# Performance work log

Hardware: AMD Instinct MI355X
Metric: run time of the kernel (lower is better)

The kernel has to match this reference:

```python
import jax, jax.numpy as jnp
import numpy as np

B, S, D = 2, 2048, 3584
H, KV, HD = 28, 4, 128
N_REP = H // KV          # 7
MAX_S = 2048
SCALE = HD ** -0.5
ROPE_BASE = 1_000_000.0  # Qwen2 rope theta


def _rope_tables(max_s, hd, base):
    inv = 1.0 / (base ** (np.arange(0, hd, 2, dtype=np.float32) / hd))  # [hd/2]
    ang = np.arange(max_s, dtype=np.float32)[:, None] * inv[None, :]    # [S, hd/2]
    return jnp.asarray(np.cos(ang)), jnp.asarray(np.sin(ang))


def apply_rotary(x, cos, sin):
    # x: [b, s, h, hd] with interleaved complex pairs (torch view_as_complex layout)
    xr = x[..., 0::2]
    xi = x[..., 1::2]
    cos = cos[None, :, None, :]
    sin = sin[None, :, None, :]
    yr = xr * cos - xi * sin
    yi = xr * sin + xi * cos
    return jnp.stack([yr, yi], axis=-1).reshape(x.shape)


def setup_inputs() -> dict:
    key = jax.random.key(0)
    ks = jax.random.split(key, 8)
    w = 0.02
    x = jax.random.normal(ks[0], (B, S, D), jnp.float32)
    wq_w = jax.random.normal(ks[1], (H * HD, D), jnp.float32) * w
    wq_b = jax.random.normal(ks[2], (H * HD,), jnp.float32) * w
    wk_w = jax.random.normal(ks[3], (KV * HD, D), jnp.float32) * w
    wk_b = jax.random.normal(ks[4], (KV * HD,), jnp.float32) * w
    wv_w = jax.random.normal(ks[5], (KV * HD, D), jnp.float32) * w
    wv_b = jax.random.normal(ks[6], (KV * HD,), jnp.float32) * w
    wo_w = jax.random.normal(ks[7], (D, H * HD), jnp.float32) * w
    k_cache = jnp.zeros((B, MAX_S, KV, HD), jnp.float32)
    v_cache = jnp.zeros((B, MAX_S, KV, HD), jnp.float32)
    freqs_cos, freqs_sin = _rope_tables(MAX_S, HD, ROPE_BASE)
    # causal additive mask [s, t]; large-negative instead of -inf for safe grads
    mask = jnp.triu(jnp.full((S, S), -1e9, jnp.float32), k=1)
    return {"x": x, "wq_w": wq_w, "wq_b": wq_b, "wk_w": wk_w, "wk_b": wk_b,
            "wv_w": wv_w, "wv_b": wv_b, "wo_w": wo_w,
            "k_cache": k_cache, "v_cache": v_cache,
            "freqs_cos": freqs_cos, "freqs_sin": freqs_sin,
            "mask": mask, "start_pos": 0}


def reference(x, wq_w, wq_b, wk_w, wk_b, wv_w, wv_b, wo_w,
              k_cache, v_cache, freqs_cos, freqs_sin, mask, start_pos):
    bsz, seqlen, _ = x.shape
    end_pos = start_pos + seqlen
    q = (x @ wq_w.T + wq_b).reshape(bsz, seqlen, H, HD)
    k = (x @ wk_w.T + wk_b).reshape(bsz, seqlen, KV, HD)
    v = (x @ wv_w.T + wv_b).reshape(bsz, seqlen, KV, HD)
    cos = jax.lax.dynamic_slice_in_dim(freqs_cos, start_pos, seqlen, 0)
    sin = jax.lax.dynamic_slice_in_dim(freqs_sin, start_pos, seqlen, 0)
    q = apply_rotary(q, cos, sin)
    k = apply_rotary(k, cos, sin)
    # KV-cache write
    k_cache = jax.lax.dynamic_update_slice(k_cache, k, (0, start_pos, 0, 0))
    v_cache = jax.lax.dynamic_update_slice(v_cache, v, (0, start_pos, 0, 0))
    keys = k_cache[:bsz, :end_pos]    # [b, t, kv, hd]
    values = v_cache[:bsz, :end_pos]
    # GQA: repeat_interleave kv heads to n_heads
    keys = jnp.repeat(keys, N_REP, axis=2)      # [b, t, h, hd]
    values = jnp.repeat(values, N_REP, axis=2)
    scores = jnp.einsum('bshd,bthd->bsht', q, keys) * SCALE
    scores = scores + mask[None, :, None, :]
    probs = jax.nn.softmax(scores.astype(jnp.float32), axis=-1).astype(x.dtype)
    out = jnp.einsum('bsht,bthd->bshd', probs, values)
    out = out.reshape(bsz, seqlen, H * HD)
    return out @ wo_w.T
```

## Files before the change

### kernel.cpp

```cpp
#include <hip/hip_runtime.h>
#include <hip/hip_bf16.h>

typedef __attribute__((ext_vector_type(4)))  float  f32x4;
typedef __attribute__((ext_vector_type(16))) float  f32x16;
typedef __attribute__((ext_vector_type(8)))  __bf16 bf16x8;
typedef __attribute__((ext_vector_type(4)))  __bf16 bf16x4;
typedef __attribute__((ext_vector_type(4)))  unsigned int u32x4;

constexpr int S_LEN = 2048, DMODEL = 3584, NH = 28, NKV = 4, HD = 128, NREP = 7;
constexpr float SCALE_LOG2 = 0.1275174331f;

__device__ __forceinline__ unsigned int pack2(float a, float b) {
  unsigned short ua = __builtin_bit_cast(unsigned short, (__bf16)a);
  unsigned short ub = __builtin_bit_cast(unsigned short, (__bf16)b);
  return (unsigned int)ua | ((unsigned int)ub << 16);
}

__global__ void cvt_kernel(const float* __restrict__ in, __bf16* __restrict__ out, int n4) {
  int i = blockIdx.x * blockDim.x + threadIdx.x;
  if (i >= n4) return;
  float4 v = reinterpret_cast<const float4*>(in)[i];
  bf16x4 o;
  o[0] = (__bf16)v.x; o[1] = (__bf16)v.y; o[2] = (__bf16)v.z; o[3] = (__bf16)v.w;
  reinterpret_cast<bf16x4*>(out)[i] = o;
}

#define GLDS16(gsrc, ldst)                                                              \
  __builtin_amdgcn_global_load_lds((const __attribute__((address_space(1))) void*)(gsrc),\
                                   (__attribute__((address_space(3))) void*)(ldst), 16, 0, 0)

template <int MODE>
__global__ __launch_bounds__(512, 2) void gemm256(
    const __bf16* __restrict__ A, const __bf16* __restrict__ Bw,
    const float* __restrict__ bias, void* __restrict__ Cout,
    int M, int N, int K,
    const float* __restrict__ fcos, const float* __restrict__ fsin,
    const int* __restrict__ sp_ptr, float scale)
{
  extern __shared__ char smem[];
  const int tid = threadIdx.x;
  const int lane = tid & 63, wid = tid >> 6;
  const int wm = wid >> 2, wn = wid & 3;
  const int l15 = lane & 15, g = (lane >> 4) & 3;

  const int chunk = gridDim.x >> 3;
  const int wg = (blockIdx.x & 7) * chunk + (blockIdx.x >> 3);
  const int nbx = N >> 8;
  const int by = wg / nbx, bx = wg % nbx;
  const int row0 = by * 256, col0 = bx * 256;

  const int srL   = 16 * (tid >> 6) + ((tid >> 2) & 15);
  const int cperm = ((tid & 3) * 8) ^ (((tid >> 5) & 1) * 16);
  const __bf16* pA0 = A + (size_t)(row0 + srL) * K + cperm;
  const __bf16* pA1 = pA0 + (size_t)128 * K;
  const __bf16* pB0 = Bw + (size_t)(col0 + srL) * K + cperm;
  const __bf16* pB1 = pB0 + (size_t)128 * K;
  char* ldsA = smem + tid * 16;
  char* ldsB = smem + 65536 + tid * 16;

  const int sw = ((l15 >> 3) & 1) << 5;
  const int aoff = wm * 8192 + l15 * 64 + ((g * 16) ^ sw);
  const int boff = 65536 + wn * 4096 + l15 * 64 + ((g * 16) ^ sw);

  f32x4 acc[8][4] = {};
  const int nt = K >> 5;

#pragma unroll
  for (int pt = 0; pt < 3; pt++) {
    const size_t ko = (size_t)pt * 32;
    char* sA = ldsA + pt * 16384;
    char* sB = ldsB + pt * 16384;
    GLDS16(pA0 + ko, sA);
    GLDS16(pA1 + ko, sA + 8192);
    GLDS16(pB0 + ko, sB);
    GLDS16(pB1 + ko, sB + 8192);
  }
  asm volatile("s_waitcnt vmcnt(8)" ::: "memory");
  __builtin_amdgcn_s_barrier();
  __builtin_amdgcn_sched_barrier(0);

  for (int t = 0; t < nt; t++) {
    const int slot = (t & 3) * 16384;
    const char* sa = smem + slot + aoff;
    const char* sb = smem + slot + boff;
    bf16x8 af[4], bfv[4];

#pragma unroll
    for (int fm = 0; fm < 4; fm++)
      af[fm] = *reinterpret_cast<const bf16x8*>(sa + fm * 1024);
#pragma unroll
    for (int fn = 0; fn < 4; fn++)
      bfv[fn] = *reinterpret_cast<const bf16x8*>(sb + fn * 1024);
    if (t + 3 < nt) {
      const size_t ko = (size_t)(t + 3) * 32;
      char* sA = ldsA + ((t + 3) & 3) * 16384;
      GLDS16(pA0 + ko, sA);
      GLDS16(pA1 + ko, sA + 8192);
    }
    asm volatile("s_waitcnt lgkmcnt(0)" ::: "memory");
    __builtin_amdgcn_sched_barrier(0);
    __builtin_amdgcn_s_setprio(1);
#pragma unroll
    for (int fn = 0; fn < 4; fn++)
#pragma unroll
      for (int fm = 0; fm < 4; fm++)
        acc[fm][fn] = __builtin_amdgcn_mfma_f32_16x16x32_bf16(af[fm], bfv[fn], acc[fm][fn], 0, 0, 0);
    __builtin_amdgcn_s_setprio(0);
    __builtin_amdgcn_s_barrier();
    __builtin_amdgcn_sched_barrier(0);

#pragma unroll
    for (int fm = 0; fm < 4; fm++)
      af[fm] = *reinterpret_cast<const bf16x8*>(sa + (4 + fm) * 1024);
    if (t + 3 < nt) {
      const size_t ko = (size_t)(t + 3) * 32;
      char* sB = ldsB + ((t + 3) & 3) * 16384;
      GLDS16(pB0 + ko, sB);
      GLDS16(pB1 + ko, sB + 8192);
    }
    asm volatile("s_waitcnt lgkmcnt(0)" ::: "memory");
    __builtin_amdgcn_sched_barrier(0);
    __builtin_amdgcn_s_setprio(1);
#pragma unroll
    for (int fn = 0; fn < 4; fn++)
#pragma unroll
      for (int fm = 0; fm < 4; fm++)
        acc[4 + fm][fn] = __builtin_amdgcn_mfma_f32_16x16x32_bf16(af[fm], bfv[fn], acc[4 + fm][fn], 0, 0, 0);
    __builtin_amdgcn_s_setprio(0);

    if (t < nt - 3)       asm volatile("s_waitcnt vmcnt(8)" ::: "memory");
    else if (t == nt - 3) asm volatile("s_waitcnt vmcnt(4)" ::: "memory");
    else if (t == nt - 2) asm volatile("s_waitcnt vmcnt(0)" ::: "memory");
    __builtin_amdgcn_s_barrier();
    __builtin_amdgcn_sched_barrier(0);
  }

  if constexpr (MODE == 0) {
    float* C = (float*)Cout;
#pragma unroll
    for (int fm = 0; fm < 8; fm++) {
      const int row = row0 + wm * 128 + fm * 16 + 4 * g;
#pragma unroll
      for (int fn = 0; fn < 4; fn++) {
        const int col = col0 + wn * 64 + fn * 16 + l15;
#pragma unroll
        for (int r = 0; r < 4; r++)
          C[(size_t)(row + r) * N + col] = acc[fm][fn][r];
      }
    }
  } else {
    __bf16* C = (__bf16*)Cout;
    const int sp = sp_ptr[0];
    float bval[4];
#pragma unroll
    for (int fn = 0; fn < 4; fn++) bval[fn] = bias[col0 + wn * 64 + fn * 16 + l15];
#pragma unroll
    for (int fm = 0; fm < 8; fm++) {
#pragma unroll
      for (int fn = 0; fn < 4; fn++) {
        const int col = col0 + wn * 64 + fn * 16 + l15;
        const int i = (col & (HD - 1)) >> 1;
#pragma unroll
        for (int r = 0; r < 4; r++) {
          const int row = row0 + wm * 128 + fm * 16 + 4 * g + r;
          float y = acc[fm][fn][r] + bval[fn];
          float p = __shfl_xor(y, 1);
          const int spos = sp + (row & (S_LEN - 1));
          const float c = fcos[spos * (HD / 2) + i];
          const float sn = fsin[spos * (HD / 2) + i];
          y = (col & 1) ? (p * sn + y * c) : (y * c - p * sn);
          C[(size_t)row * N + col] = (__bf16)(y * scale);
        }
      }
    }
  }
}

__global__ __launch_bounds__(256) void gemm_kv(
    const __bf16* __restrict__ A,
    const __bf16* __restrict__ Wk, const float* __restrict__ bk, __bf16* __restrict__ Ko,
    const __bf16* __restrict__ Wv, const float* __restrict__ bv, __bf16* __restrict__ Vo,
    const float* __restrict__ fcos, const float* __restrict__ fsin,
    const int* __restrict__ sp_ptr)
{
  constexpr int N = 512, K = 3584;
  __shared__ __bf16 As[128 * 32];
  __shared__ __bf16 Bs[128 * 32];
  const int tid = threadIdx.x;
  const int lane = tid & 63, wid = tid >> 6;
  const int l15 = lane & 15, g = lane >> 4;
  const int wr = wid >> 1, wc = wid & 1;
  const bool isK = blockIdx.x < 4;
  const __bf16* Bw = isK ? Wk : Wv;
  const float* bias = isK ? bk : bv;
  __bf16* Cout = isK ? Ko : Vo;
  const int row0 = blockIdx.y * 128;
  const int col0 = (blockIdx.x & 3) * 128;

  f32x4 acc[4][4] = {};

  const int srow = tid >> 2;
  const int scol = (tid & 3) * 8;
  const __bf16* Ag0 = A + (size_t)(row0 + srow) * K + scol;
  const __bf16* Ag1 = Ag0 + (size_t)64 * K;
  const __bf16* Bg0 = Bw + (size_t)(col0 + srow) * K + scol;
  const __bf16* Bg1 = Bg0 + (size_t)64 * K;
  __bf16* As0 = As + tid * 8;
  __bf16* As1 = As + 2048 + tid * 8;
  __bf16* Bs0 = Bs + tid * 8;
  __bf16* Bs1 = Bs + 2048 + tid * 8;

  for (int k0 = 0; k0 < K; k0 += 32) {
    GLDS16(Ag0 + k0, As0);
    GLDS16(Ag1 + k0, As1);
    GLDS16(Bg0 + k0, Bs0);
    GLDS16(Bg1 + k0, Bs1);
    __syncthreads();
    bf16x8 af[4], bfr[4];
#pragma unroll
    for (int m = 0; m < 4; m++)
      af[m] = *reinterpret_cast<const bf16x8*>(As + (wr * 64 + m * 16 + l15) * 32 + g * 8);
#pragma unroll
    for (int n = 0; n < 4; n++)
      bfr[n] = *reinterpret_cast<const bf16x8*>(Bs + (wc * 64 + n * 16 + l15) * 32 + g * 8);
#pragma unroll
    for (int m = 0; m < 4; m++)
#pragma unroll
      for (int n = 0; n < 4; n++)
        acc[m][n] = __builtin_amdgcn_mfma_f32_16x16x32_bf16(af[m], bfr[n], acc[m][n], 0, 0, 0);
    __syncthreads();
  }

  const int sp = sp_ptr[0];
#pragma unroll
  for (int m = 0; m < 4; m++) {
#pragma unroll
    for (int n = 0; n < 4; n++) {
      const int col = col0 + wc * 64 + n * 16 + l15;
      const float bval = bias[col];
      f32x4 v = acc[m][n];
#pragma unroll
      for (int r = 0; r < 4; r++) {
        const int row = row0 + wr * 64 + m * 16 + 4 * g + r;
        float y = v[r] + bval;
        if (isK) {
          float p = __shfl_xor(y, 1);
          const int i = (col & (HD - 1)) >> 1;
          const int spos = sp + (row & (S_LEN - 1));
          const float c = fcos[spos * (HD / 2) + i];
          const float sn = fsin[spos * (HD / 2) + i];
          y = (col & 1) ? (p * sn + y * c) : (y * c - p * sn);
        }
        Cout[(size_t)row * N + col] = (__bf16)y;
      }
    }
  }
}

__global__ void vtrans_kernel(const __bf16* __restrict__ Vg, __bf16* __restrict__ Vt) {
  __shared__ __bf16 t[32][33];
  const int bkv = blockIdx.z;
  const int b = bkv >> 2, kv = bkv & 3;
  const int s0 = blockIdx.x * 32, h0 = blockIdx.y * 32;
  const int tid = threadIdx.x;
#pragma unroll
  for (int c = 0; c < 4; c++) {
    int idx = c * 256 + tid;
    int sr = idx >> 5, hc = idx & 31;
    t[sr][hc] = Vg[(((size_t)b * S_LEN + s0 + sr) * NKV + kv) * HD + h0 + hc];
  }
  __syncthreads();
#pragma unroll
  for (int c = 0; c < 4; c++) {
    int idx = c * 256 + tid;
    int hr = idx >> 5, sc = idx & 31;
    Vt[(((size_t)b * NKV + kv) * HD + h0 + hr) * S_LEN + s0 + sc] = t[sc][hr];
  }
}

__global__ __launch_bounds__(256, 2) void attn_kernel(
    const __bf16* __restrict__ Qb, const __bf16* __restrict__ Kb,
    const __bf16* __restrict__ Vt, __bf16* __restrict__ Ob)
{
  __shared__ __align__(16) char asmem[65536];

  const int tid = threadIdx.x, lane = tid & 63, wid = tid >> 6;
  const int l31 = lane & 31, hh = lane >> 5;
  const int b = blockIdx.z, h = blockIdx.y;
  const int kvh = h / NREP;
  const int qi = 15 - blockIdx.x;
  const int qw = qi * 128 + wid * 32;
  const int qg = qw + l31;

  bf16x8 qf[8];
  {
    const __bf16* qp = Qb + (((size_t)b * S_LEN + qg) * NH + h) * HD + hh * 8;
#pragma unroll
    for (int c = 0; c < 8; c++) qf[c] = *reinterpret_cast<const bf16x8*>(qp + c * 16);
  }

  f32x16 o[4] = {};
  float mrun = -3.0e38f, lsum = 0.0f;

  const __bf16* Kbase = Kb + ((size_t)b * S_LEN * NKV + kvh) * HD;
  const __bf16* Vbase = Vt + ((size_t)b * NKV + kvh) * (size_t)HD * S_LEN;

  const int trow = tid >> 4;
  const int kcol = (((tid & 15) * 16) ^ ((trow & 7) << 4)) >> 1;
  const int vrow = tid >> 3;
  const int vcol = (((tid & 7) * 16) ^ ((vrow & 7) << 4)) >> 1;

  const int ntiles = 2 * qi + 2;

#define STAGE(T, S)                                                                     \
  do {                                                                                  \
    const int k0_ = (T) * 64;                                                           \
    char* Kd_ = asmem + (S) * 32768;                                                    \
    char* Vd_ = Kd_ + 16384;                                                            \
    _Pragma("unroll")                                                                   \
    for (int p = 0; p < 4; p++) {                                                       \
      GLDS16(Kbase + (size_t)(k0_ + p * 16 + trow) * (NKV * HD) + kcol,                 \
             Kd_ + (p * 256 + tid) * 16);                                               \
      GLDS16(Vbase + (size_t)(p * 32 + vrow) * S_LEN + k0_ + vcol,                      \
             Vd_ + (p * 256 + tid) * 16);                                               \
    }                                                                                   \
  } while (0)

  STAGE(0, 0);

  for (int t = 0; t < ntiles; t++) {
    __syncthreads();
    if (t + 1 < ntiles) STAGE(t + 1, (t + 1) & 1);

    const char* Ksb = asmem + (t & 1) * 32768;
    const char* Vsb = Ksb + 16384;
    const int k0 = t * 64;

    f32x16 s0 = {}, s1 = {};
    {
      const char* kp0 = Ksb + l31 * 256;
      const char* kp1 = kp0 + 32 * 256;
      const int sw = (l31 & 7) << 4;
      __builtin_amdgcn_s_setprio(1);
#pragma unroll
      for (int c = 0; c < 8; c++) {
        const int cb = (c * 32 + hh * 16) ^ sw;
        bf16x8 kf0 = *reinterpret_cast<const bf16x8*>(kp0 + cb);
        s0 = __builtin_amdgcn_mfma_f32_32x32x16_bf16(kf0, qf[c], s0, 0, 0, 0);
        bf16x8 kf1 = *reinterpret_cast<const bf16x8*>(kp1 + cb);
        s1 = __builtin_amdgcn_mfma_f32_32x32x16_bf16(kf1, qf[c], s1, 0, 0, 0);
      }
      __builtin_amdgcn_s_setprio(0);
    }

    if (k0 + 63 > qw) {
#pragma unroll
      for (int r = 0; r < 16; r++) {
        const int kvo = k0 + ((r & 3) + 8 * (r >> 2)) + 4 * hh;
        if (kvo > qg)      s0[r] = -1.0e9f;
        if (kvo + 32 > qg) s1[r] = -1.0e9f;
      }
    }

    float pmax = -3.0e38f;
#pragma unroll
    for (int r = 0; r < 16; r++) { pmax = fmaxf(pmax, s0[r]); pmax = fmaxf(pmax, s1[r]); }
    pmax = fmaxf(pmax, __shfl_xor(pmax, 32));
    if (!__all(pmax <= mrun + 11.5f)) {
      const float mnew = fmaxf(mrun, pmax);
      const float fs = exp2f(mrun - mnew);
      lsum *= fs;
#pragma unroll
      for (int dt = 0; dt < 4; dt++) o[dt] *= fs;
      mrun = mnew;
    }
    float psum = 0.0f;
#pragma unroll
    for (int r = 0; r < 16; r++) {
      s0[r] = exp2f(s0[r] - mrun); psum += s0[r];
      s1[r] = exp2f(s1[r] - mrun); psum += s1[r];
    }
    lsum += psum;

    unsigned int pk[2][8], px[2][8];
#pragma unroll
    for (int j = 0; j < 8; j++) {
      pk[0][j] = pack2(s0[2 * j], s0[2 * j + 1]);
      pk[1][j] = pack2(s1[2 * j], s1[2 * j + 1]);
    }
#pragma unroll
    for (int tt = 0; tt < 2; tt++)
#pragma unroll
      for (int j = 0; j < 8; j++) px[tt][j] = __shfl_xor(pk[tt][j], 32);

    __builtin_amdgcn_s_setprio(1);
#pragma unroll
    for (int tt = 0; tt < 2; tt++) {
#pragma unroll
      for (int c2 = 0; c2 < 2; c2++) {
        u32x4 pb4;
        if (hh == 0)
          pb4 = (u32x4){pk[tt][4 * c2], pk[tt][4 * c2 + 1], px[tt][4 * c2], px[tt][4 * c2 + 1]};
        else
          pb4 = (u32x4){px[tt][4 * c2 + 2], px[tt][4 * c2 + 3], pk[tt][4 * c2 + 2], pk[tt][4 * c2 + 3]};
        bf16x8 pbf = __builtin_bit_cast(bf16x8, pb4);
        const int colb = tt * 64 + c2 * 32 + hh * 16;
#pragma unroll
        for (int dt = 0; dt < 4; dt++) {
          const int d = dt * 32 + l31;
          bf16x8 vf = *reinterpret_cast<const bf16x8*>(Vsb + d * 128 + (colb ^ ((d & 7) << 4)));
          o[dt] = __builtin_amdgcn_mfma_f32_32x32x16_bf16(vf, pbf, o[dt], 0, 0, 0);
        }
      }
    }
    __builtin_amdgcn_s_setprio(0);
  }
#undef STAGE

  lsum += __shfl_xor(lsum, 32);
  const float inv = 1.0f / lsum;
  char* my = asmem + wid * 8192;
#pragma unroll
  for (int dt = 0; dt < 4; dt++) {
#pragma unroll
    for (int j = 0; j < 8; j++) {
      const int r = 2 * j;
      const int d = dt * 32 + ((r & 3) + 8 * (r >> 2)) + 4 * hh;
      const unsigned int w = pack2(o[dt][r] * inv, o[dt][r + 1] * inv);
      *reinterpret_cast<unsigned int*>(my + ((l31 * 256 + d * 2) ^ ((l31 & 7) << 4))) = w;
    }
  }
#pragma unroll
  for (int j = 0; j < 8; j++) {
    const int idx = j * 64 + lane;
    const int row = idx >> 4, c16 = idx & 15;
    u32x4 val = *reinterpret_cast<u32x4*>(my + row * 256 + ((c16 * 16) ^ ((row & 7) << 4)));
    *reinterpret_cast<u32x4*>(Ob + (size_t)(b * S_LEN + qw + row) * (NH * HD) + h * HD + c16 * 8) = val;
  }
}

extern "C" void kernel_launch(void* const* d_in, const int* in_sizes, int n_in,
                              void* d_out, int out_size, void* d_ws, size_t ws_size,
                              hipStream_t stream) {
  (void)in_sizes; (void)n_in; (void)out_size; (void)ws_size;
  const float* x    = (const float*)d_in[0];
  const float* wq_w = (const float*)d_in[1];
  const float* wq_b = (const float*)d_in[2];
  const float* wk_w = (const float*)d_in[3];
  const float* wk_b = (const float*)d_in[4];
  const float* wv_w = (const float*)d_in[5];
  const float* wv_b = (const float*)d_in[6];
  const float* wo_w = (const float*)d_in[7];
  const float* fcos = (const float*)d_in[10];
  const float* fsin = (const float*)d_in[11];
  const int*   spp  = (const int*)d_in[13];
  float* out = (float*)d_out;

  constexpr size_t XB_N = (size_t)4096 * 3584;
  constexpr size_t WQ_N = (size_t)3584 * 3584;
  constexpr size_t WK_N = (size_t)512 * 3584;
  constexpr size_t WO_N = (size_t)3584 * 3584;
  constexpr size_t KB_N = (size_t)4096 * 512;

  __bf16* xb  = (__bf16*)d_ws;
  __bf16* wqb = xb + XB_N;
  __bf16* wkb = wqb + WQ_N;
  __bf16* wvb = wkb + WK_N;
  __bf16* wob = wvb + WK_N;
  __bf16* Qb  = wob + WO_N;
  __bf16* Kb  = Qb + XB_N;
  __bf16* Vg  = Kb + KB_N;
  __bf16* Vt  = Vg + KB_N;
  __bf16* Ob  = xb;

  auto cvt = [&](const float* src, __bf16* dst, size_t n) {
    int n4 = (int)(n / 4);
    cvt_kernel<<<(n4 + 255) / 256, 256, 0, stream>>>(src, dst, n4);
  };
  cvt(x, xb, XB_N);
  cvt(wq_w, wqb, WQ_N);
  cvt(wk_w, wkb, WK_N);
  cvt(wv_w, wvb, WK_N);
  cvt(wo_w, wob, WO_N);

  gemm256<2><<<dim3(224), 512, 131072, stream>>>(xb, wqb, wq_b, Qb, 4096, 3584, 3584,
                                                 fcos, fsin, spp, SCALE_LOG2);
  gemm_kv<<<dim3(8, 32), 256, 0, stream>>>(xb, wkb, wk_b, Kb, wvb, wv_b, Vg,
                                           fcos, fsin, spp);
  vtrans_kernel<<<dim3(64, 4, 8), 256, 0, stream>>>(Vg, Vt);
  attn_kernel<<<dim3(16, 28, 2), 256, 0, stream>>>(Qb, Kb, Vt, Ob);
  gemm256<0><<<dim3(224), 512, 131072, stream>>>(Ob, wob, nullptr, out, 4096, 3584, 3584,
                                                 nullptr, nullptr, nullptr, 1.0f);
}
```

Baseline: 519.2 us.

## Make attention kernel persistent with atomic work queue in longest-first order

The attention kernel becomes persistent. It launches 512 blocks, and each block repeatedly pulls a (query tile, head, batch) item from a global atomic counter until all 896 items are done. Items are ordered so the longest causal query tiles across all heads and batches are taken first. The aim is to balance load across CUs for the triangular causal workload and to shrink the tail. The cost is an extra tiny kernel to zero the counter, plus one atomic and one barrier per item.

```diff
diff --git a/kernel.cpp b/kernel.cpp
--- a/kernel.cpp
+++ b/kernel.cpp
@@ -24,6 +24,8 @@
   o[0] = (__bf16)v.x; o[1] = (__bf16)v.y; o[2] = (__bf16)v.z; o[3] = (__bf16)v.w;
   reinterpret_cast<bf16x4*>(out)[i] = o;
 }
+
+__global__ void zero_ctr_kernel(int* p) { *p = 0; }
 
 #define GLDS16(gsrc, ldst)                                                              \
   __builtin_amdgcn_global_load_lds((const __attribute__((address_space(1))) void*)(gsrc),\
@@ -280,162 +282,174 @@
 
 __global__ __launch_bounds__(256, 2) void attn_kernel(
     const __bf16* __restrict__ Qb, const __bf16* __restrict__ Kb,
-    const __bf16* __restrict__ Vt, __bf16* __restrict__ Ob)
+    const __bf16* __restrict__ Vt, __bf16* __restrict__ Ob, int* __restrict__ ctr)
 {
   __shared__ __align__(16) char asmem[65536];
+  __shared__ int jsh;
 
   const int tid = threadIdx.x, lane = tid & 63, wid = tid >> 6;
   const int l31 = lane & 31, hh = lane >> 5;
-  const int b = blockIdx.z, h = blockIdx.y;
-  const int kvh = h / NREP;
-  const int qi = 15 - blockIdx.x;
-  const int qw = qi * 128 + wid * 32;
-  const int qg = qw + l31;
-
-  bf16x8 qf[8];
-  {
-    const __bf16* qp = Qb + (((size_t)b * S_LEN + qg) * NH + h) * HD + hh * 8;
-#pragma unroll
-    for (int c = 0; c < 8; c++) qf[c] = *reinterpret_cast<const bf16x8*>(qp + c * 16);
-  }
-
-  f32x16 o[4] = {};
-  float mrun = -3.0e38f, lsum = 0.0f;
-
-  const __bf16* Kbase = Kb + ((size_t)b * S_LEN * NKV + kvh) * HD;
-  const __bf16* Vbase = Vt + ((size_t)b * NKV + kvh) * (size_t)HD * S_LEN;
 
   const int trow = tid >> 4;
   const int kcol = (((tid & 15) * 16) ^ ((trow & 7) << 4)) >> 1;
   const int vrow = tid >> 3;
   const int vcol = (((tid & 7) * 16) ^ ((vrow & 7) << 4)) >> 1;
 
-  const int ntiles = 2 * qi + 2;
+  constexpr int NITEMS = 16 * NH * 2;
+
+  while (true) {
+    if (tid == 0) jsh = atomicAdd(ctr, 1);
+    __syncthreads();
+    const int j = jsh;
+    if (j >= NITEMS) break;
+
+    const int qi = 15 - (j / 56);
+    const int r56 = j % 56;
+    const int h = r56 >> 1, b = r56 & 1;
+    const int kvh = h / NREP;
+    const int qw = qi * 128 + wid * 32;
+    const int qg = qw + l31;
+
+    const __bf16* Kbase = Kb + ((size_t)b * S_LEN * NKV + kvh) * HD;
+    const __bf16* Vbase = Vt + ((size_t)b * NKV + kvh) * (size_t)HD * S_LEN;
+
+    bf16x8 qf[8];
+    {
+      const __bf16* qp = Qb + (((size_t)b * S_LEN + qg) * NH + h) * HD + hh * 8;
+#pragma unroll
+      for (int c = 0; c < 8; c++) qf[c] = *reinterpret_cast<const bf16x8*>(qp + c * 16);
+    }
+
+    f32x16 o[4] = {};
+    float mrun = -3.0e38f, lsum = 0.0f;
+
+    const int ntiles = 2 * qi + 2;
 
 #define STAGE(T, S)                                                                     \
-  do {                                                                                  \
-    const int k0_ = (T) * 64;                                                           \
-    char* Kd_ = asmem + (S) * 32768;                                                    \
-    char* Vd_ = Kd_ + 16384;                                                            \
-    _Pragma("unroll")                                                                   \
-    for (int p = 0; p < 4; p++) {                                                       \
-      GLDS16(Kbase + (size_t)(k0_ + p * 16 + trow) * (NKV * HD) + kcol,                 \
-             Kd_ + (p * 256 + tid) * 16);                                               \
-      GLDS16(Vbase + (size_t)(p * 32 + vrow) * S_LEN + k0_ + vcol,                      \
-             Vd_ + (p * 256 + tid) * 16);                                               \
-    }                                                                                   \
-  } while (0)
-
-  STAGE(0, 0);
-
-  for (int t = 0; t < ntiles; t++) {
-    __syncthreads();
-    if (t + 1 < ntiles) STAGE(t + 1, (t + 1) & 1);
-
-    const char* Ksb = asmem + (t & 1) * 32768;
-    const char* Vsb = Ksb + 16384;
-    const int k0 = t * 64;
-
-    f32x16 s0 = {}, s1 = {};
-    {
-      const char* kp0 = Ksb + l31 * 256;
-      const char* kp1 = kp0 + 32 * 256;
-      const int sw = (l31 & 7) << 4;
+    do {                                                                                \
+      const int k0_ = (T) * 64;                                                         \
+      char* Kd_ = asmem + (S) * 32768;                                                  \
+      char* Vd_ = Kd_ + 16384;                                                          \
+      _Pragma("unroll")                                                                 \
+      for (int p = 0; p < 4; p++) {                                                     \
+        GLDS16(Kbase + (size_t)(k0_ + p * 16 + trow) * (NKV * HD) + kcol,               \
+               Kd_ + (p * 256 + tid) * 16);                                             \
+        GLDS16(Vbase + (size_t)(p * 32 + vrow) * S_LEN + k0_ + vcol,                    \
+               Vd_ + (p * 256 + tid) * 16);                                             \
+      }                                                                                 \
+    } while (0)
+
+    STAGE(0, 0);
+
+    for (int t = 0; t < ntiles; t++) {
+      __syncthreads();
+      if (t + 1 < ntiles) STAGE(t + 1, (t + 1) & 1);
+
+      const char* Ksb = asmem + (t & 1) * 32768;
+      const char* Vsb = Ksb + 16384;
+      const int k0 = t * 64;
+
+      f32x16 s0 = {}, s1 = {};
+      {
+        const char* kp0 = Ksb + l31 * 256;
+        const char* kp1 = kp0 + 32 * 256;
+        const int sw = (l31 & 7) << 4;
+        __builtin_amdgcn_s_setprio(1);
+#pragma unroll
+        for (int c = 0; c < 8; c++) {
+          const int cb = (c * 32 + hh * 16) ^ sw;
+          bf16x8 kf0 = *reinterpret_cast<const bf16x8*>(kp0 + cb);
+          s0 = __builtin_amdgcn_mfma_f32_32x32x16_bf16(kf0, qf[c], s0, 0, 0, 0);
+          bf16x8 kf1 = *reinterpret_cast<const bf16x8*>(kp1 + cb);
+          s1 = __builtin_amdgcn_mfma_f32_32x32x16_bf16(kf1, qf[c], s1, 0, 0, 0);
+        }
+        __builtin_amdgcn_s_setprio(0);
+      }
+
+      if (k0 + 63 > qw) {
+#pragma unroll
+        for (int r = 0; r < 16; r++) {
+          const int kvo = k0 + ((r & 3) + 8 * (r >> 2)) + 4 * hh;
+          if (kvo > qg)      s0[r] = -1.0e9f;
+          if (kvo + 32 > qg) s1[r] = -1.0e9f;
+        }
+      }
+
+      float pmax = -3.0e38f;
+#pragma unroll
+      for (int r = 0; r < 16; r++) { pmax = fmaxf(pmax, s0[r]); pmax = fmaxf(pmax, s1[r]); }
+      pmax = fmaxf(pmax, __shfl_xor(pmax, 32));
+      if (!__all(pmax <= mrun + 11.5f)) {
+        const float mnew = fmaxf(mrun, pmax);
+        const float fs = exp2f(mrun - mnew);
+        lsum *= fs;
+#pragma unroll
+        for (int dt = 0; dt < 4; dt++) o[dt] *= fs;
+        mrun = mnew;
+      }
+      float psum = 0.0f;
+#pragma unroll
+      for (int r = 0; r < 16; r++) {
+        s0[r] = exp2f(s0[r] - mrun); psum += s0[r];
+        s1[r] = exp2f(s1[r] - mrun); psum += s1[r];
+      }
+      lsum += psum;
+
+      unsigned int pk[2][8], px[2][8];
+#pragma unroll
+      for (int jj = 0; jj < 8; jj++) {
+        pk[0][jj] = pack2(s0[2 * jj], s0[2 * jj + 1]);
+        pk[1][jj] = pack2(s1[2 * jj], s1[2 * jj + 1]);
+      }
+#pragma unroll
+      for (int tt = 0; tt < 2; tt++)
+#pragma unroll
+        for (int jj = 0; jj < 8; jj++) px[tt][jj] = __shfl_xor(pk[tt][jj], 32);
+
       __builtin_amdgcn_s_setprio(1);
 #pragma unroll
-      for (int c = 0; c < 8; c++) {
-        const int cb = (c * 32 + hh * 16) ^ sw;
-        bf16x8 kf0 = *reinterpret_cast<const bf16x8*>(kp0 + cb);
-        s0 = __builtin_amdgcn_mfma_f32_32x32x16_bf16(kf0, qf[c], s0, 0, 0, 0);
-        bf16x8 kf1 = *reinterpret_cast<const bf16x8*>(kp1 + cb);
-        s1 = __builtin_amdgcn_mfma_f32_32x32x16_bf16(kf1, qf[c], s1, 0, 0, 0);
+      for (int tt = 0; tt < 2; tt++) {
+#pragma unroll
+        for (int c2 = 0; c2 < 2; c2++) {
+          u32x4 pb4;
+          if (hh == 0)
+            pb4 = (u32x4){pk[tt][4 * c2], pk[tt][4 * c2 + 1], px[tt][4 * c2], px[tt][4 * c2 + 1]};
+          else
+            pb4 = (u32x4){px[tt][4 * c2 + 2], px[tt][4 * c2 + 3], pk[tt][4 * c2 + 2], pk[tt][4 * c2 + 3]};
+          bf16x8 pbf = __builtin_bit_cast(bf16x8, pb4);
+          const int colb = tt * 64 + c2 * 32 + hh * 16;
+#pragma unroll
+          for (int dt = 0; dt < 4; dt++) {
+            const int d = dt * 32 + l31;
+            bf16x8 vf = *reinterpret_cast<const bf16x8*>(Vsb + d * 128 + (colb ^ ((d & 7) << 4)));
+            o[dt] = __builtin_amdgcn_mfma_f32_32x32x16_bf16(vf, pbf, o[dt], 0, 0, 0);
+          }
+        }
       }
       __builtin_amdgcn_s_setprio(0);
     }
-
-    if (k0 + 63 > qw) {
-#pragma unroll
-      for (int r = 0; r < 16; r++) {
-        const int kvo = k0 + ((r & 3) + 8 * (r >> 2)) + 4 * hh;
-        if (kvo > qg)      s0[r] = -1.0e9f;
-        if (kvo + 32 > qg) s1[r] = -1.0e9f;
-      }
-    }
-
-    float pmax = -3.0e38f;
-#pragma unroll
-    for (int r = 0; r < 16; r++) { pmax = fmaxf(pmax, s0[r]); pmax = fmaxf(pmax, s1[r]); }
-    pmax = fmaxf(pmax, __shfl_xor(pmax, 32));
-    if (!__all(pmax <= mrun + 11.5f)) {
-      const float mnew = fmaxf(mrun, pmax);
-      const float fs = exp2f(mrun - mnew);
-      lsum *= fs;
-#pragma unroll
-      for (int dt = 0; dt < 4; dt++) o[dt] *= fs;
-      mrun = mnew;
-    }
-    float psum = 0.0f;
-#pragma unroll
-    for (int r = 0; r < 16; r++) {
-      s0[r] = exp2f(s0[r] - mrun); psum += s0[r];
-      s1[r] = exp2f(s1[r] - mrun); psum += s1[r];
-    }
-    lsum += psum;
-
-    unsigned int pk[2][8], px[2][8];
-#pragma unroll
-    for (int j = 0; j < 8; j++) {
-      pk[0][j] = pack2(s0[2 * j], s0[2 * j + 1]);
-      pk[1][j] = pack2(s1[2 * j], s1[2 * j + 1]);
-    }
-#pragma unroll
-    for (int tt = 0; tt < 2; tt++)
-#pragma unroll
-      for (int j = 0; j < 8; j++) px[tt][j] = __shfl_xor(pk[tt][j], 32);
-
-    __builtin_amdgcn_s_setprio(1);
-#pragma unroll
-    for (int tt = 0; tt < 2; tt++) {
-#pragma unroll
-      for (int c2 = 0; c2 < 2; c2++) {
-        u32x4 pb4;
-        if (hh == 0)
-          pb4 = (u32x4){pk[tt][4 * c2], pk[tt][4 * c2 + 1], px[tt][4 * c2], px[tt][4 * c2 + 1]};
-        else
-          pb4 = (u32x4){px[tt][4 * c2 + 2], px[tt][4 * c2 + 3], pk[tt][4 * c2 + 2], pk[tt][4 * c2 + 3]};
-        bf16x8 pbf = __builtin_bit_cast(bf16x8, pb4);
-        const int colb = tt * 64 + c2 * 32 + hh * 16;
-#pragma unroll
-        for (int dt = 0; dt < 4; dt++) {
-          const int d = dt * 32 + l31;
-          bf16x8 vf = *reinterpret_cast<const bf16x8*>(Vsb + d * 128 + (colb ^ ((d & 7) << 4)));
-          o[dt] = __builtin_amdgcn_mfma_f32_32x32x16_bf16(vf, pbf, o[dt], 0, 0, 0);
-        }
-      }
-    }
-    __builtin_amdgcn_s_setprio(0);
-  }
 #undef STAGE
 
-  lsum += __shfl_xor(lsum, 32);
-  const float inv = 1.0f / lsum;
-  char* my = asmem + wid * 8192;
-#pragma unroll
-  for (int dt = 0; dt < 4; dt++) {
-#pragma unroll
-    for (int j = 0; j < 8; j++) {
-      const int r = 2 * j;
-      const int d = dt * 32 + ((r & 3) + 8 * (r >> 2)) + 4 * hh;
-      const unsigned int w = pack2(o[dt][r] * inv, o[dt][r + 1] * inv);
-      *reinterpret_cast<unsigned int*>(my + ((l31 * 256 + d * 2) ^ ((l31 & 7) << 4))) = w;
-    }
-  }
-#pragma unroll
-  for (int j = 0; j < 8; j++) {
-    const int idx = j * 64 + lane;
-    const int row = idx >> 4, c16 = idx & 15;
-    u32x4 val = *reinterpret_cast<u32x4*>(my + row * 256 + ((c16 * 16) ^ ((row & 7) << 4)));
-    *reinterpret_cast<u32x4*>(Ob + (size_t)(b * S_LEN + qw + row) * (NH * HD) + h * HD + c16 * 8) = val;
+    lsum += __shfl_xor(lsum, 32);
+    const float inv = 1.0f / lsum;
+    char* my = asmem + wid * 8192;
+#pragma unroll
+    for (int dt = 0; dt < 4; dt++) {
+#pragma unroll
+      for (int jj = 0; jj < 8; jj++) {
+        const int r = 2 * jj;
+        const int d = dt * 32 + ((r & 3) + 8 * (r >> 2)) + 4 * hh;
+        const unsigned int w = pack2(o[dt][r] * inv, o[dt][r + 1] * inv);
+        *reinterpret_cast<unsigned int*>(my + ((l31 * 256 + d * 2) ^ ((l31 & 7) << 4))) = w;
+      }
+    }
+#pragma unroll
+    for (int jj = 0; jj < 8; jj++) {
+      const int idx = jj * 64 + lane;
+      const int row = idx >> 4, c16 = idx & 15;
+      u32x4 val = *reinterpret_cast<u32x4*>(my + row * 256 + ((c16 * 16) ^ ((row & 7) << 4)));
+      *reinterpret_cast<u32x4*>(Ob + (size_t)(b * S_LEN + qw + row) * (NH * HD) + h * HD + c16 * 8) = val;
+    }
   }
 }
 
@@ -471,6 +485,7 @@
   __bf16* Kb  = Qb + XB_N;
   __bf16* Vg  = Kb + KB_N;
   __bf16* Vt  = Vg + KB_N;
+  int*    ctr = (int*)(Vt + KB_N);
   __bf16* Ob  = xb;
 
   auto cvt = [&](const float* src, __bf16* dst, size_t n) {
@@ -482,13 +497,14 @@
   cvt(wk_w, wkb, WK_N);
   cvt(wv_w, wvb, WK_N);
   cvt(wo_w, wob, WO_N);
+  zero_ctr_kernel<<<1, 1, 0, stream>>>(ctr);
 
   gemm256<2><<<dim3(224), 512, 131072, stream>>>(xb, wqb, wq_b, Qb, 4096, 3584, 3584,
                                                  fcos, fsin, spp, SCALE_LOG2);
   gemm_kv<<<dim3(8, 32), 256, 0, stream>>>(xb, wkb, wk_b, Kb, wvb, wv_b, Vg,
                                            fcos, fsin, spp);
   vtrans_kernel<<<dim3(64, 4, 8), 256, 0, stream>>>(Vg, Vt);
-  attn_kernel<<<dim3(16, 28, 2), 256, 0, stream>>>(Qb, Kb, Vt, Ob);
+  attn_kernel<<<dim3(512), 256, 0, stream>>>(Qb, Kb, Vt, Ob, ctr);
   gemm256<0><<<dim3(224), 512, 131072, stream>>>(Ob, wob, nullptr, out, 4096, 3584, 3584,
                                                  nullptr, nullptr, nullptr, 1.0f);
 }
```

Measured after the change: 450.8 us. -13.2%, faster.
